# Kernel tuning notes

Measured on AMD Instinct MI355X. Metric: run time of the kernel, lower is better.

## Reference

```python
import jax, jax.numpy as jnp
import numpy as np

N, T, D, H = 128, 64, 1024, 1024
DA = 4  # hard-coded 4x4 attention grid


def setup_inputs() -> dict:
    key = jax.random.key(0)
    ks = jax.random.split(key, 6)
    x = jax.random.normal(ks[0], (N, T, D), dtype=jnp.float32)
    A = jax.random.normal(ks[1], (N, H, DA, DA), dtype=jnp.float32)
    Wx = jax.random.normal(ks[2], (D, 4 * H), dtype=jnp.float32) / np.sqrt(D)
    Wh = jax.random.normal(ks[3], (H, 4 * H), dtype=jnp.float32) / np.sqrt(H)
    Wattn = jax.random.normal(ks[4], (H, 4 * H), dtype=jnp.float32) / np.sqrt(H)
    b = jnp.zeros((4 * H,), dtype=jnp.float32)
    return {"x": x, "A": A, "Wx": Wx, "Wh": Wh, "Wattn": Wattn, "b": b}


def reference(x, A, Wx, Wh, Wattn, b):
    n, h_dim, da, _ = A.shape
    Af = A.reshape(n, h_dim, da * da)          # (N, H, P) with P = 16
    h0 = A.mean(axis=(2, 3))                   # global image feature init
    c0 = h0
    scale = jnp.sqrt(jnp.asarray(h_dim, x.dtype))

    def step(carry, xt):
        h, c = carry
        # scaled dot-product attention over P=16 spatial positions
        scores = jnp.einsum('nh,nhp->np', h, Af) / scale   # (N, P)
        w = jax.nn.softmax(scores, axis=1)
        attn = jnp.einsum('nhp,np->nh', Af, w)             # (N, H)
        # fused LSTM gates
        act = xt @ Wx + h @ Wh + attn @ Wattn + b          # (N, 4H)
        i, f, o, g = jnp.split(act, 4, axis=1)
        i = jax.nn.sigmoid(i)
        f = jax.nn.sigmoid(f)
        o = jax.nn.sigmoid(o)
        g = jnp.tanh(g)
        c_next = f * c + i * g
        h_next = o * jnp.tanh(c_next)
        return (h_next, c_next), h_next

    _, hs = jax.lax.scan(step, (h0, c0), jnp.swapaxes(x, 0, 1))  # (T, N, H)
    return jnp.swapaxes(hs, 0, 1)                                # (N, T, H)
```

## Files before the change

kernel.cpp:

```cpp
#include <hip/hip_runtime.h>
#include <hip/hip_bf16.h>
#include <cmath>

#define N_   128
#define T_   64
#define D_   1024
#define H_   1024
#define G4_  4096

typedef short bf16x8 __attribute__((ext_vector_type(8)));
typedef float f32x4  __attribute__((ext_vector_type(4)));

__device__ __forceinline__ unsigned short f2bf(float f) {
    union { float f; unsigned int u; } v; v.f = f;
    unsigned int r = (v.u + 0x7FFFu + ((v.u >> 16) & 1u)) >> 16;
    return (unsigned short)r;
}
__device__ __forceinline__ float bf2f(unsigned short s) {
    union { unsigned int u; float f; } v; v.u = ((unsigned int)s) << 16;
    return v.f;
}



__global__ void k_pack_w(const float* __restrict__ src, unsigned short* __restrict__ dst,
                         int kcoff, int kctot) {
    __shared__ float ld[64][33];
    int j0 = blockIdx.x * 32, k0 = blockIdx.y * 64;
    int tid = threadIdx.x;
    int c = tid & 31, r = tid >> 5;
    #pragma unroll
    for (int i = 0; i < 8; i++)
        ld[r + i * 8][c] = src[(long)(k0 + r + i * 8) * G4_ + j0 + c];
    __syncthreads();
    int j = tid & 31, ku = tid >> 5;
    int kcl = ku >> 2, kg = ku & 3;
    int jti = (j0 + j) >> 4, cl = (j0 + j) & 15;
    int kc = kcoff + (k0 >> 5) + kcl;
    unsigned short q[8];
    #pragma unroll
    for (int e = 0; e < 8; e++) q[e] = f2bf(ld[ku * 8 + e][j]);
    *(uint4*)(dst + ((long)(jti * kctot + kc) * 64 + kg * 16 + cl) * 8) = *(uint4*)q;
}

__global__ void k_pack_x2(const float* __restrict__ x, unsigned short* __restrict__ xP) {
    long gid = (long)blockIdx.x * 256 + threadIdx.x;
    int m = (int)(gid >> 7), u = (int)(gid & 127);
    const float* src = x + (long)m * 1024 + u * 8;
    int n = m >> 6, t = m & 63;
    int tile = t * 8 + (n >> 4);
    int kc = u >> 2, kg = u & 3, cl = n & 15;
    float4 a = *(const float4*)src, b = *(const float4*)(src + 4);
    unsigned short q[8] = {f2bf(a.x), f2bf(a.y), f2bf(a.z), f2bf(a.w),
                           f2bf(b.x), f2bf(b.y), f2bf(b.z), f2bf(b.w)};
    *(uint4*)(xP + ((long)(tile * 32 + kc) * 64 + kg * 16 + cl) * 8) = *(uint4*)q;
}

__global__ void k_pack_af(const float* __restrict__ A, unsigned short* __restrict__ AfP,
                          unsigned short* __restrict__ Af2) {
    __shared__ float ld[64][17];
    int n = blockIdx.x, h0 = blockIdx.y * 64;
    int tid = threadIdx.x;
    int hh = tid >> 2, pq = tid & 3;
    float4 v = *(const float4*)(A + ((long)n * H_ + h0 + hh) * 16 + pq * 4);
    unsigned short o[4] = {f2bf(v.x), f2bf(v.y), f2bf(v.z), f2bf(v.w)};
    *(uint2*)(Af2 + ((long)n * H_ + h0 + hh) * 16 + pq * 4) = *(uint2*)o;
    ld[hh][pq * 4 + 0] = v.x; ld[hh][pq * 4 + 1] = v.y;
    ld[hh][pq * 4 + 2] = v.z; ld[hh][pq * 4 + 3] = v.w;
    __syncthreads();
    if (tid < 128) {
        int p = tid >> 3, ku = tid & 7;
        int kc = (h0 >> 5) + (ku >> 2), kg = ku & 3;
        unsigned short q[8];
        #pragma unroll
        for (int e = 0; e < 8; e++) q[e] = f2bf(ld[ku * 8 + e][p]);
        *(uint4*)(AfP + ((long)(n * 32 + kc) * 64 + kg * 16 + p) * 8) = *(uint4*)q;
    }
}

__global__ void k_h0(const float* __restrict__ A, float* __restrict__ h,
                     float* __restrict__ c, unsigned short* __restrict__ hP0) {
    long id = (long)blockIdx.x * 256 + threadIdx.x;
    const float4* ap = (const float4*)(A + id * 16);
    float s = 0.f;
    #pragma unroll
    for (int q = 0; q < 4; q++) { float4 v = ap[q]; s += v.x + v.y + v.z + v.w; }
    float m = s * (1.0f / 16.0f);
    h[id] = m; c[id] = m;
    int n = (int)(id >> 10), j = (int)(id & 1023);
    hP0[((long)((n >> 4) * 32 + (j >> 5)) * 64 + ((j >> 3) & 3) * 16 + (n & 15)) * 8 + (j & 7)] = f2bf(m);
}

__global__ __launch_bounds__(512)
void k_part0(const float* __restrict__ hbuf, const unsigned short* __restrict__ Af2,
             float* __restrict__ partial0) {
    int n = blockIdx.x;
    int tid = threadIdx.x;
    int jh = tid * 2;
    float sp[16];
    #pragma unroll
    for (int p = 0; p < 16; p++) sp[p] = 0.f;
    #pragma unroll
    for (int u = 0; u < 2; u++) {
        float hv = hbuf[(long)n * H_ + jh + u];
        const unsigned short* afp = Af2 + ((long)n * H_ + jh + u) * 16;
        bf16x8 a0 = *(const bf16x8*)(afp);
        bf16x8 a1 = *(const bf16x8*)(afp + 8);
        #pragma unroll
        for (int p = 0; p < 8; p++) { sp[p] += hv * bf2f((unsigned short)a0[p]);
                                      sp[8+p] += hv * bf2f((unsigned short)a1[p]); }
    }
    #pragma unroll
    for (int off = 1; off < 8; off <<= 1) {
        #pragma unroll
        for (int p = 0; p < 16; p++) sp[p] += __shfl_xor(sp[p], off);
    }
    int jt = tid >> 3;
    if ((tid & 7) == 0) {
        #pragma unroll
        for (int p = 0; p < 16; p++)
            partial0[((long)n * 16 + p) * 64 + jt] = sp[p];
    }
}

__global__ __launch_bounds__(64)
void k_score_tiny(const float* __restrict__ partial, float* __restrict__ wbuf) {
    int n = blockIdx.x;
    int lane = threadIdx.x;
    int p = lane & 15, c4 = lane >> 4;
    const float* src = partial + ((long)n * 16 + p) * 64 + c4 * 16;
    float s = 0.f;
    #pragma unroll
    for (int q = 0; q < 16; q++) s += src[q];
    s += __shfl_xor(s, 16);
    s += __shfl_xor(s, 32);
    s *= (1.0f / 32.0f);
    float m = s;
    #pragma unroll
    for (int off = 1; off < 16; off <<= 1) m = fmaxf(m, __shfl_xor(m, off));
    float e = expf(s - m);
    float sum = e;
    #pragma unroll
    for (int off = 1; off < 16; off <<= 1) sum += __shfl_xor(sum, off);
    if (c4 == 0) wbuf[n * 16 + p] = e / sum;
}

__global__ __launch_bounds__(256, 2)
void k_aw(const unsigned short* __restrict__ AfP, const unsigned short* __restrict__ WattnP,
          unsigned short* __restrict__ AW) {
    int tid = threadIdx.x;
    int wv = tid >> 6, lane = tid & 63;
    int wr = wv >> 1, wc = wv & 1;
    int cl = lane & 15, kg = lane >> 4;
    int at0 = blockIdx.x * 8 + wr * 4;
    int jt0 = blockIdx.y * 8 + wc * 4;

    f32x4 acc[4][4];
    #pragma unroll
    for (int i = 0; i < 4; i++)
        #pragma unroll
        for (int j = 0; j < 4; j++) acc[i][j] = (f32x4){0.f, 0.f, 0.f, 0.f};

    const unsigned short* apx[4];
    const unsigned short* bpx[4];
    #pragma unroll
    for (int i = 0; i < 4; i++) {
        apx[i] = AfP    + (long)(at0 + i) * (32 * 512) + lane * 8;
        bpx[i] = WattnP + (long)(jt0 + i) * (32 * 512) + lane * 8;
    }
    #pragma unroll 2
    for (int kc = 0; kc < 32; kc++) {
        bf16x8 a[4], b[4];
        #pragma unroll
        for (int i = 0; i < 4; i++) a[i] = *(const bf16x8*)(apx[i] + kc * 512);
        #pragma unroll
        for (int i = 0; i < 4; i++) b[i] = *(const bf16x8*)(bpx[i] + kc * 512);
        #pragma unroll
        for (int i = 0; i < 4; i++)
            #pragma unroll
            for (int j = 0; j < 4; j++)
                acc[i][j] = __builtin_amdgcn_mfma_f32_16x16x32_bf16(a[i], b[j], acc[i][j], 0, 0, 0);
    }
    #pragma unroll
    for (int i = 0; i < 4; i++) {
        int n = at0 + i;
        #pragma unroll
        for (int j = 0; j < 4; j++) {
            int jj = (jt0 + j) * 16 + cl;
            #pragma unroll
            for (int v = 0; v < 4; v++) {
                int p = kg * 4 + v;
                AW[((long)n * G4_ + jj) * 16 + p] = f2bf(acc[i][j][v]);
            }
        }
    }
}

__global__ __launch_bounds__(256, 2)
void k_actx(const unsigned short* __restrict__ xP, const unsigned short* __restrict__ WxP,
            unsigned short* __restrict__ actx) {
    int tid = threadIdx.x;
    int wv = tid >> 6, lane = tid & 63;
    int wr = wv >> 1, wc = wv & 1;
    int cl = lane & 15, kg = lane >> 4;
    int at0 = blockIdx.x * 8 + wr * 4;
    int jt0 = blockIdx.y * 8 + wc * 4;

    f32x4 acc[4][4];
    #pragma unroll
    for (int i = 0; i < 4; i++)
        #pragma unroll
        for (int j = 0; j < 4; j++) acc[i][j] = (f32x4){0.f, 0.f, 0.f, 0.f};

    const unsigned short* apx[4];
    const unsigned short* bpx[4];
    #pragma unroll
    for (int i = 0; i < 4; i++) {
        apx[i] = xP  + (long)(at0 + i) * (32 * 512) + lane * 8;
        bpx[i] = WxP + (long)(jt0 + i) * (32 * 512) + lane * 8;
    }
    #pragma unroll 2
    for (int kc = 0; kc < 32; kc++) {
        bf16x8 a[4], b[4];
        #pragma unroll
        for (int i = 0; i < 4; i++) a[i] = *(const bf16x8*)(apx[i] + kc * 512);
        #pragma unroll
        for (int i = 0; i < 4; i++) b[i] = *(const bf16x8*)(bpx[i] + kc * 512);
        #pragma unroll
        for (int i = 0; i < 4; i++)
            #pragma unroll
            for (int j = 0; j < 4; j++)
                acc[i][j] = __builtin_amdgcn_mfma_f32_16x16x32_bf16(a[i], b[j], acc[i][j], 0, 0, 0);
    }
    #pragma unroll
    for (int i = 0; i < 4; i++) {
        long mrow = (long)(at0 + i) * 16;
        #pragma unroll
        for (int j = 0; j < 4; j++) {
            int jj = (jt0 + j) * 16 + cl;
            #pragma unroll
            for (int v = 0; v < 4; v++)
                actx[(mrow + kg * 4 + v) * G4_ + jj] = f2bf(acc[i][j][v]);
        }
    }
}


__global__ __launch_bounds__(512, 2)
void k_step(const unsigned short* __restrict__ actx,
            const unsigned short* __restrict__ hPin,
            unsigned short* __restrict__ hPout,
            const unsigned short* __restrict__ WhP,
            const unsigned short* __restrict__ AW,
            const unsigned short* __restrict__ Af2,
            const float* __restrict__ wbuf,
            const float* __restrict__ bvec,
            float* __restrict__ c,
            float* __restrict__ partOUT,
            float* __restrict__ out, int t) {
    int tid = threadIdx.x;
    int wv = tid >> 6, lane = tid & 63;
    int ks = wv & 3, rh = wv >> 2;
    int cl = lane & 15, kg = lane >> 4;
    int jt = blockIdx.x;
    int nt2 = blockIdx.y;
    int colbase = jt * 16;

    f32x4 acc[4];
    #pragma unroll
    for (int g = 0; g < 4; g++) acc[g] = (f32x4){0.f, 0.f, 0.f, 0.f};

    const unsigned short* abase = hPin + ((long)(nt2 * 2 + rh) * 32 + ks * 8) * 512 + lane * 8;
    const unsigned short* bb[4];
    #pragma unroll
    for (int g = 0; g < 4; g++)
        bb[g] = WhP + ((long)(g * 64 + jt) * 32 + ks * 8) * 512 + lane * 8;

    #pragma unroll
    for (int i = 0; i < 8; i++) {
        bf16x8 a = *(const bf16x8*)(abase + i * 512);
        #pragma unroll
        for (int g = 0; g < 4; g++) {
            bf16x8 b = *(const bf16x8*)(bb[g] + i * 512);
            acc[g] = __builtin_amdgcn_mfma_f32_16x16x32_bf16(a, b, acc[g], 0, 0, 0);
        }
    }

    __shared__ float red[3][2][64][17];
    __shared__ float act[4][32][17];
    if (ks != 0) {
        #pragma unroll
        for (int g = 0; g < 4; g++)
            #pragma unroll
            for (int v = 0; v < 4; v++) red[ks - 1][rh][lane][g * 4 + v] = acc[g][v];
    }
    __syncthreads();
    if (ks == 0) {
        #pragma unroll
        for (int g = 0; g < 4; g++)
            #pragma unroll
            for (int v = 0; v < 4; v++) {
                float s = acc[g][v] + red[0][rh][lane][g*4+v] + red[1][rh][lane][g*4+v]
                        + red[2][rh][lane][g*4+v];
                act[g][rh * 16 + kg * 4 + v][cl] = s;
            }
    }
    __syncthreads();

    int nloc = tid >> 4, jl = tid & 15;
    int n = nt2 * 32 + nloc, jh = colbase + jl;
    float wv16[16];
    #pragma unroll
    for (int p = 0; p < 16; p++) wv16[p] = wbuf[n * 16 + p];

    long rm = (long)(t * 8 + (n >> 4)) * 16 + (n & 15);
    float s4[4];
    #pragma unroll
    for (int g = 0; g < 4; g++) {
        int j = g * 1024 + jh;
        const unsigned short* awp = AW + ((long)n * G4_ + j) * 16;
        bf16x8 aw0 = *(const bf16x8*)(awp);
        bf16x8 aw1 = *(const bf16x8*)(awp + 8);
        float at = 0.f;
        #pragma unroll
        for (int p = 0; p < 8; p++) at += wv16[p]     * bf2f((unsigned short)aw0[p]);
        #pragma unroll
        for (int p = 0; p < 8; p++) at += wv16[8 + p] * bf2f((unsigned short)aw1[p]);
        s4[g] = act[g][nloc][jl] + bf2f(actx[rm * G4_ + j]) + at + bvec[j];
    }
    float ig = 1.f / (1.f + expf(-s4[0]));
    float fg = 1.f / (1.f + expf(-s4[1]));
    float og = 1.f / (1.f + expf(-s4[2]));
    float gg = tanhf(s4[3]);
    long idx = (long)n * H_ + jh;
    float cn = fg * c[idx] + ig * gg;
    float hn = og * tanhf(cn);
    c[idx] = cn;
    out[((long)n * T_ + t) * H_ + jh] = hn;
    hPout[((long)((n >> 4) * 32 + (jh >> 5)) * 64 + ((jh >> 3) & 3) * 16 + (n & 15)) * 8 + (jh & 7)] = f2bf(hn);

    const unsigned short* afp = Af2 + ((long)n * H_ + jh) * 16;
    bf16x8 af0 = *(const bf16x8*)(afp);
    bf16x8 af1 = *(const bf16x8*)(afp + 8);
    float sp[16];
    #pragma unroll
    for (int p = 0; p < 8; p++) { sp[p]     = hn * bf2f((unsigned short)af0[p]);
                                  sp[8 + p] = hn * bf2f((unsigned short)af1[p]); }
    #pragma unroll
    for (int off = 1; off < 16; off <<= 1) {
        #pragma unroll
        for (int p = 0; p < 16; p++) sp[p] += __shfl_xor(sp[p], off);
    }
    float outv = 0.f;
    #pragma unroll
    for (int p = 0; p < 16; p++) if (jl == p) outv = sp[p];
    partOUT[((long)n * 16 + jl) * 64 + jt] = outv;
}


extern "C" void kernel_launch(void* const* d_in, const int* in_sizes, int n_in,
                              void* d_out, int out_size, void* d_ws, size_t ws_size,
                              hipStream_t stream) {
    const float* x     = (const float*)d_in[0];
    const float* A     = (const float*)d_in[1];
    const float* Wx    = (const float*)d_in[2];
    const float* Wh    = (const float*)d_in[3];
    const float* Wattn = (const float*)d_in[4];
    const float* b     = (const float*)d_in[5];
    float* out = (float*)d_out;

    char* ws = (char*)d_ws;
    size_t off = 0;
    auto alloc = [&](size_t bytes) -> void* {
        void* p = ws + off;
        off += (bytes + 255) & ~(size_t)255;
        return p;
    };
    unsigned short* xP     = (unsigned short*)alloc((size_t)512 * 32 * 512 * 2);
    unsigned short* WxP    = (unsigned short*)alloc((size_t)256 * 32 * 512 * 2);
    unsigned short* WhP    = (unsigned short*)alloc((size_t)256 * 32 * 512 * 2);
    unsigned short* WattnP = (unsigned short*)alloc((size_t)256 * 32 * 512 * 2);
    unsigned short* AfP    = (unsigned short*)alloc((size_t)128 * 32 * 512 * 2);
    unsigned short* Af2    = (unsigned short*)alloc((size_t)N_ * H_ * 16 * 2);
    unsigned short* AW     = (unsigned short*)alloc((size_t)N_ * G4_ * 16 * 2);
    unsigned short* actx   = (unsigned short*)alloc((size_t)8192 * G4_ * 2);
    float*          hbuf   = (float*)alloc((size_t)N_ * H_ * 4);
    float*          cbuf   = (float*)alloc((size_t)N_ * H_ * 4);
    unsigned short* hP0    = (unsigned short*)alloc((size_t)8 * 32 * 512 * 2);
    unsigned short* hP1    = (unsigned short*)alloc((size_t)8 * 32 * 512 * 2);
    float*          part0  = (float*)alloc((size_t)N_ * 16 * 64 * 4);
    float*          part1  = (float*)alloc((size_t)N_ * 16 * 64 * 4);
    float*          wbuf   = (float*)alloc((size_t)N_ * 16 * 4);

    k_pack_w<<<dim3(128, 16), dim3(256), 0, stream>>>(Wx,    WxP,    0, 32);
    k_pack_w<<<dim3(128, 16), dim3(256), 0, stream>>>(Wh,    WhP,    0, 32);
    k_pack_w<<<dim3(128, 16), dim3(256), 0, stream>>>(Wattn, WattnP, 0, 32);
    k_pack_x2<<<dim3(4096), dim3(256), 0, stream>>>(x, xP);
    k_pack_af<<<dim3(128, 16), dim3(256), 0, stream>>>(A, AfP, Af2);
    k_h0<<<dim3(512), dim3(256), 0, stream>>>(A, hbuf, cbuf, hP0);
    k_part0<<<dim3(N_), dim3(512), 0, stream>>>(hbuf, Af2, part0);
    k_aw<<<dim3(16, 32), dim3(256), 0, stream>>>(AfP, WattnP, AW);
    k_actx<<<dim3(64, 32), dim3(256), 0, stream>>>(xP, WxP, actx);

    for (int t = 0; t < T_; t++) {
        unsigned short* hin  = (t & 1) ? hP1 : hP0;
        unsigned short* hout = (t & 1) ? hP0 : hP1;
        float* pIN  = (t & 1) ? part1 : part0;
        float* pOUT = (t & 1) ? part0 : part1;
        k_score_tiny<<<dim3(N_), dim3(64), 0, stream>>>(pIN, wbuf);
        k_step<<<dim3(64, 4), dim3(512), 0, stream>>>(actx, hin, hout, WhP, AW, Af2,
                                                      wbuf, b, cbuf, pOUT, out, t);
    }
}
```

Before: 1.044 ms.

## Fuse attention softmax into step kernel and widen actx GEMM tile

Removes the separate per-timestep softmax kernel. Each step block now recomputes the softmax weights for its 32 rows from the partial scores and keeps them in shared memory, which drops 64 kernel launches and the wbuf global round trip. The cost is redundant softmax work across the 64 column blocks. The precompute x@Wx GEMM also changes to an 8x4 MFMA tile per wave with half the grid, giving more A-operand reuse but more registers per thread.

```diff
diff --git a/kernel.cpp b/kernel.cpp
--- a/kernel.cpp
+++ b/kernel.cpp
@@ -123,28 +123,6 @@
     }
 }
 
-__global__ __launch_bounds__(64)
-void k_score_tiny(const float* __restrict__ partial, float* __restrict__ wbuf) {
-    int n = blockIdx.x;
-    int lane = threadIdx.x;
-    int p = lane & 15, c4 = lane >> 4;
-    const float* src = partial + ((long)n * 16 + p) * 64 + c4 * 16;
-    float s = 0.f;
-    #pragma unroll
-    for (int q = 0; q < 16; q++) s += src[q];
-    s += __shfl_xor(s, 16);
-    s += __shfl_xor(s, 32);
-    s *= (1.0f / 32.0f);
-    float m = s;
-    #pragma unroll
-    for (int off = 1; off < 16; off <<= 1) m = fmaxf(m, __shfl_xor(m, off));
-    float e = expf(s - m);
-    float sum = e;
-    #pragma unroll
-    for (int off = 1; off < 16; off <<= 1) sum += __shfl_xor(sum, off);
-    if (c4 == 0) wbuf[n * 16 + p] = e / sum;
-}
-
 __global__ __launch_bounds__(256, 2)
 void k_aw(const unsigned short* __restrict__ AfP, const unsigned short* __restrict__ WattnP,
           unsigned short* __restrict__ AW) {
@@ -201,39 +179,38 @@
             unsigned short* __restrict__ actx) {
     int tid = threadIdx.x;
     int wv = tid >> 6, lane = tid & 63;
-    int wr = wv >> 1, wc = wv & 1;
     int cl = lane & 15, kg = lane >> 4;
-    int at0 = blockIdx.x * 8 + wr * 4;
-    int jt0 = blockIdx.y * 8 + wc * 4;
-
-    f32x4 acc[4][4];
-    #pragma unroll
-    for (int i = 0; i < 4; i++)
+    int at0 = blockIdx.x * 8;
+    int jt0 = blockIdx.y * 16 + wv * 4;
+
+    f32x4 acc[8][4];
+    #pragma unroll
+    for (int i = 0; i < 8; i++)
         #pragma unroll
         for (int j = 0; j < 4; j++) acc[i][j] = (f32x4){0.f, 0.f, 0.f, 0.f};
 
-    const unsigned short* apx[4];
+    const unsigned short* apx[8];
     const unsigned short* bpx[4];
     #pragma unroll
-    for (int i = 0; i < 4; i++) {
-        apx[i] = xP  + (long)(at0 + i) * (32 * 512) + lane * 8;
-        bpx[i] = WxP + (long)(jt0 + i) * (32 * 512) + lane * 8;
-    }
-    #pragma unroll 2
+    for (int i = 0; i < 8; i++) apx[i] = xP  + (long)(at0 + i) * (32 * 512) + lane * 8;
+    #pragma unroll
+    for (int j = 0; j < 4; j++) bpx[j] = WxP + (long)(jt0 + j) * (32 * 512) + lane * 8;
+
+    #pragma unroll 1
     for (int kc = 0; kc < 32; kc++) {
-        bf16x8 a[4], b[4];
-        #pragma unroll
-        for (int i = 0; i < 4; i++) a[i] = *(const bf16x8*)(apx[i] + kc * 512);
-        #pragma unroll
-        for (int i = 0; i < 4; i++) b[i] = *(const bf16x8*)(bpx[i] + kc * 512);
-        #pragma unroll
-        for (int i = 0; i < 4; i++)
+        bf16x8 a[8], b[4];
+        #pragma unroll
+        for (int i = 0; i < 8; i++) a[i] = *(const bf16x8*)(apx[i] + kc * 512);
+        #pragma unroll
+        for (int j = 0; j < 4; j++) b[j] = *(const bf16x8*)(bpx[j] + kc * 512);
+        #pragma unroll
+        for (int i = 0; i < 8; i++)
             #pragma unroll
             for (int j = 0; j < 4; j++)
                 acc[i][j] = __builtin_amdgcn_mfma_f32_16x16x32_bf16(a[i], b[j], acc[i][j], 0, 0, 0);
     }
     #pragma unroll
-    for (int i = 0; i < 4; i++) {
+    for (int i = 0; i < 8; i++) {
         long mrow = (long)(at0 + i) * 16;
         #pragma unroll
         for (int j = 0; j < 4; j++) {
@@ -253,10 +230,10 @@
             const unsigned short* __restrict__ WhP,
             const unsigned short* __restrict__ AW,
             const unsigned short* __restrict__ Af2,
-            const float* __restrict__ wbuf,
+            const float* __restrict__ partIN,
+            float* __restrict__ partOUT,
             const float* __restrict__ bvec,
             float* __restrict__ c,
-            float* __restrict__ partOUT,
             float* __restrict__ out, int t) {
     int tid = threadIdx.x;
     int wv = tid >> 6, lane = tid & 63;
@@ -266,6 +243,28 @@
     int nt2 = blockIdx.y;
     int colbase = jt * 16;
 
+    __shared__ float wsm[32][17];
+    __shared__ float red[3][2][64][17];
+    __shared__ float act[4][32][17];
+
+    {
+        int nloc = tid >> 4, p = tid & 15;
+        int n = nt2 * 32 + nloc;
+        const float* src = partIN + ((long)n * 16 + p) * 64;
+        float s = 0.f;
+        #pragma unroll 8
+        for (int q = 0; q < 64; q++) s += src[q];
+        s *= (1.0f / 32.0f);
+        float m = s;
+        #pragma unroll
+        for (int off = 1; off < 16; off <<= 1) m = fmaxf(m, __shfl_xor(m, off));
+        float e = expf(s - m);
+        float sum = e;
+        #pragma unroll
+        for (int off = 1; off < 16; off <<= 1) sum += __shfl_xor(sum, off);
+        wsm[nloc][p] = e / sum;
+    }
+
     f32x4 acc[4];
     #pragma unroll
     for (int g = 0; g < 4; g++) acc[g] = (f32x4){0.f, 0.f, 0.f, 0.f};
@@ -286,8 +285,6 @@
         }
     }
 
-    __shared__ float red[3][2][64][17];
-    __shared__ float act[4][32][17];
     if (ks != 0) {
         #pragma unroll
         for (int g = 0; g < 4; g++)
@@ -311,7 +308,7 @@
     int n = nt2 * 32 + nloc, jh = colbase + jl;
     float wv16[16];
     #pragma unroll
-    for (int p = 0; p < 16; p++) wv16[p] = wbuf[n * 16 + p];
+    for (int p = 0; p < 16; p++) wv16[p] = wsm[nloc][p];
 
     long rm = (long)(t * 8 + (n >> 4)) * 16 + (n & 15);
     float s4[4];
@@ -390,7 +387,6 @@
     unsigned short* hP1    = (unsigned short*)alloc((size_t)8 * 32 * 512 * 2);
     float*          part0  = (float*)alloc((size_t)N_ * 16 * 64 * 4);
     float*          part1  = (float*)alloc((size_t)N_ * 16 * 64 * 4);
-    float*          wbuf   = (float*)alloc((size_t)N_ * 16 * 4);
 
     k_pack_w<<<dim3(128, 16), dim3(256), 0, stream>>>(Wx,    WxP,    0, 32);
     k_pack_w<<<dim3(128, 16), dim3(256), 0, stream>>>(Wh,    WhP,    0, 32);
@@ -400,15 +396,14 @@
     k_h0<<<dim3(512), dim3(256), 0, stream>>>(A, hbuf, cbuf, hP0);
     k_part0<<<dim3(N_), dim3(512), 0, stream>>>(hbuf, Af2, part0);
     k_aw<<<dim3(16, 32), dim3(256), 0, stream>>>(AfP, WattnP, AW);
-    k_actx<<<dim3(64, 32), dim3(256), 0, stream>>>(xP, WxP, actx);
+    k_actx<<<dim3(64, 16), dim3(256), 0, stream>>>(xP, WxP, actx);
 
     for (int t = 0; t < T_; t++) {
         unsigned short* hin  = (t & 1) ? hP1 : hP0;
         unsigned short* hout = (t & 1) ? hP0 : hP1;
         float* pIN  = (t & 1) ? part1 : part0;
         float* pOUT = (t & 1) ? part0 : part1;
-        k_score_tiny<<<dim3(N_), dim3(64), 0, stream>>>(pIN, wbuf);
         k_step<<<dim3(64, 4), dim3(512), 0, stream>>>(actx, hin, hout, WhP, AW, Af2,
-                                                      wbuf, b, cbuf, pOUT, out, t);
-    }
-}
+                                                      pIN, pOUT, b, cbuf, out, t);
+    }
+}
```

Result: slower. 1.157 ms (+10.8%).
